# Kernel optimization log

Hardware: AMD Instinct MI355X
Metric: run time of the kernel (lower is better)

The kernel has to match this reference:

```python
import jax, jax.numpy as jnp
import numpy as np

EPS = 1e-8  # torch cosine_similarity default eps


def setup_inputs() -> dict:
    key = jax.random.key(0)
    x = jax.random.normal(key, (256, 200, 1024), dtype=jnp.float32)
    return {"x": x}


def reference(x):
    # x: [B, c, l]
    # Cosine-similarity Gram matrix, fused: dot(i,j) / max(||x_i||*||x_j||, eps)
    norms = jnp.linalg.norm(x, axis=-1)                      # [B, c]
    dots = jnp.einsum('bil,bjl->bij', x, x)                  # [B, c, c]
    sim = dots / jnp.maximum(norms[:, :, None] * norms[:, None, :], EPS)
    atten = jax.nn.softmax(sim, axis=-1)                     # [B, c, c]
    out = jnp.einsum('bij,bjl->bil', atten, x) + x           # bmm + residual
    return out
```

## Files before the change

kernel.cpp:

```cpp
#include <hip/hip_runtime.h>
#include <math.h>


typedef unsigned int uint32;
typedef __attribute__((ext_vector_type(8))) short bf16x8;
typedef __attribute__((ext_vector_type(4))) float f32x4;
typedef __attribute__((ext_vector_type(4))) uint32 u32x4;

#define CC 200
#define LL 1024
#define EPSV 1e-8f

__device__ __forceinline__ uint32 bfb(float f) {
  uint32 u = __float_as_uint(f);
  u += 0x7fffu + ((u >> 16) & 1u);
  return u >> 16;
}

__global__ __launch_bounds__(512, 2)
void spe_attn_kernel(const float* __restrict__ x, float* __restrict__ out) {
  const int tid  = threadIdx.x;
  const int lane = tid & 63;
  const int w    = tid >> 6;
  const int lm   = lane & 15;
  const int lg   = lane >> 4;
  const int bidx = blockIdx.x;
  const float* xb = x + (size_t)bidx * (CC * LL);
  float* ob       = out + (size_t)bidx * (CC * LL);

  __shared__ uint32 LDS[39120];
  uint32* pl    = LDS;
  uint32* xa0   = LDS + 24128;
  uint32* xa1   = LDS + 31616;
  uint32* xbuf  = LDS + 24128;
  float*  norms = (float*)(LDS + 38912);

  const bool two = (w < 5);
  const int rb0 = w;
  const int rb1 = two ? (w + 8) : w;

  const f32x4 fz = {0.f, 0.f, 0.f, 0.f};
  f32x4 acc[2][13];
  #pragma unroll
  for (int i = 0; i < 2; ++i)
    #pragma unroll
    for (int j = 0; j < 13; ++j) acc[i][j] = fz;

  if (tid < 288) { xa0[7200 + tid] = 0u; xa1[7200 + tid] = 0u; }

  float4 vst[7];
  #pragma unroll
  for (int i = 0; i < 7; ++i) {
    int idx = tid + i * 512;
    if (idx < 3200) {
      int row = idx >> 4, c4 = idx & 15;
      vst[i] = *(const float4*)(xb + row * LL + c4 * 4);
    }
  }
  #pragma unroll
  for (int i = 0; i < 7; ++i) {
    int idx = tid + i * 512;
    if (idx < 3200) {
      int row = idx >> 4, c4 = idx & 15;
      uint2 wv;
      wv.x = bfb(vst[i].x) | (bfb(vst[i].y) << 16);
      wv.y = bfb(vst[i].z) | (bfb(vst[i].w) << 16);
      *(uint2*)&xa0[row * 36 + c4 * 2] = wv;
    }
  }

  for (int s = 0; s < 16; ++s) {
    __syncthreads();
    if (s + 1 < 16) {
      #pragma unroll
      for (int i = 0; i < 7; ++i) {
        int idx = tid + i * 512;
        if (idx < 3200) {
          int row = idx >> 4, c4 = idx & 15;
          vst[i] = *(const float4*)(xb + row * LL + (s + 1) * 64 + c4 * 4);
        }
      }
    }
    const uint32* cur = (s & 1) ? xa1 : xa0;
    #pragma unroll
    for (int ks = 0; ks < 2; ++ks) {
      bf16x8 a0 = *(const bf16x8*)&cur[(rb0 * 16 + lm) * 36 + ks * 16 + lg * 4];
      bf16x8 a1 = a0;
      if (two) a1 = *(const bf16x8*)&cur[(rb1 * 16 + lm) * 36 + ks * 16 + lg * 4];
      #pragma unroll
      for (int ct = 0; ct < 13; ++ct) {
        bf16x8 bf = *(const bf16x8*)&cur[(ct * 16 + lm) * 36 + ks * 16 + lg * 4];
        acc[0][ct] = __builtin_amdgcn_mfma_f32_16x16x32_bf16(a0, bf, acc[0][ct], 0, 0, 0);
        if (two)
          acc[1][ct] = __builtin_amdgcn_mfma_f32_16x16x32_bf16(a1, bf, acc[1][ct], 0, 0, 0);
      }
    }
    if (s + 1 < 16) {
      uint32* nxt = (s & 1) ? xa0 : xa1;
      #pragma unroll
      for (int i = 0; i < 7; ++i) {
        int idx = tid + i * 512;
        if (idx < 3200) {
          int row = idx >> 4, c4 = idx & 15;
          uint2 wv;
          wv.x = bfb(vst[i].x) | (bfb(vst[i].y) << 16);
          wv.y = bfb(vst[i].z) | (bfb(vst[i].w) << 16);
          *(uint2*)&nxt[row * 36 + c4 * 2] = wv;
        }
      }
    }
  }

  #pragma unroll
  for (int rbi = 0; rbi < 2; ++rbi) {
    if (rbi == 0 || two) {
      int rb = rbi ? rb1 : rb0;
      #pragma unroll
      for (int ct = 0; ct < 13; ++ct) {
        if (ct == rb) {
          #pragma unroll
          for (int r = 0; r < 4; ++r) {
            int ri = lg * 4 + r;
            if (lm == ri) norms[rb * 16 + ri] = sqrtf(acc[rbi][ct][r]);
          }
        }
      }
    }
  }
  __syncthreads();

  float cn[13];
  #pragma unroll
  for (int ct = 0; ct < 13; ++ct) cn[ct] = norms[ct * 16 + lm];

  #pragma unroll
  for (int rbi = 0; rbi < 2; ++rbi) {
    if (rbi == 0 || two) {
      int rb = rbi ? rb1 : rb0;
      #pragma unroll
      for (int r = 0; r < 4; ++r) {
        int grow = rb * 16 + lg * 4 + r;
        float rn = norms[grow];
        float sv[13];
        float m = -INFINITY;
        #pragma unroll
        for (int ct = 0; ct < 13; ++ct) {
          int gc = ct * 16 + lm;
          float sval = acc[rbi][ct][r] / fmaxf(rn * cn[ct], EPSV);
          sval = (gc < CC) ? sval : -INFINITY;
          sv[ct] = sval;
          m = fmaxf(m, sval);
        }
        #pragma unroll
        for (int off = 1; off < 16; off <<= 1) m = fmaxf(m, __shfl_xor(m, off));
        float sum = 0.f;
        #pragma unroll
        for (int ct = 0; ct < 13; ++ct) {
          float e = __expf(sv[ct] - m);
          sv[ct] = e;
          sum += e;
        }
        #pragma unroll
        for (int off = 1; off < 16; off <<= 1) sum += __shfl_xor(sum, off);
        float inv = 1.0f / sum;
        #pragma unroll
        for (int ct = 0; ct < 13; ++ct) {
          int gc = ct * 16 + lm;
          float p = sv[ct] * inv + ((gc == grow) ? 1.0f : 0.0f);
          uint32 pb = bfb(p);
          uint32 qb = (uint32)__shfl_xor((int)pb, 1);
          if (!(lane & 1)) pl[grow * 116 + ct * 8 + (lm >> 1)] = pb | (qb << 16);
        }
      }
      for (int i = lane; i < 256; i += 64)
        pl[(rb * 16 + (i >> 4)) * 116 + 100 + (i & 15)] = 0u;
    }
  }

  for (int nc = 0; nc < 8; ++nc) {
    const int n0 = nc * 128;
    __syncthreads();
    #pragma unroll
    for (int pass = 0; pass < 14; ++pass) {
      int kp = pass * 8 + w;
      int r0 = kp * 2, r1 = r0 + 1;
      int n = n0 + (lane << 1);
      float2 va = (r0 < CC) ? *(const float2*)(xb + r0 * LL + n) : make_float2(0.f, 0.f);
      float2 vb = (r1 < CC) ? *(const float2*)(xb + r1 * LL + n) : make_float2(0.f, 0.f);
      uint2 wv;
      wv.x = bfb(va.x) | (bfb(vb.x) << 16);
      wv.y = bfb(va.y) | (bfb(vb.y) << 16);
      *(uint2*)&xbuf[kp * 132 + (lane << 1)] = wv;
    }
    __syncthreads();

    f32x4 acc2[2][8];
    #pragma unroll
    for (int i = 0; i < 2; ++i)
      #pragma unroll
      for (int j = 0; j < 8; ++j) acc2[i][j] = fz;

    #pragma unroll
    for (int ks = 0; ks < 7; ++ks) {
      bf16x8 a0 = *(const bf16x8*)&pl[(rb0 * 16 + lm) * 116 + ks * 16 + lg * 4];
      bf16x8 a1 = a0;
      if (two) a1 = *(const bf16x8*)&pl[(rb1 * 16 + lm) * 116 + ks * 16 + lg * 4];
      #pragma unroll
      for (int ct = 0; ct < 8; ++ct) {
        int kpb = ks * 16 + lg * 4;
        int col = ct * 16 + lm;
        u32x4 bv;
        bv[0] = xbuf[(kpb + 0) * 132 + col];
        bv[1] = xbuf[(kpb + 1) * 132 + col];
        bv[2] = xbuf[(kpb + 2) * 132 + col];
        bv[3] = xbuf[(kpb + 3) * 132 + col];
        bf16x8 bf = __builtin_bit_cast(bf16x8, bv);
        acc2[0][ct] = __builtin_amdgcn_mfma_f32_16x16x32_bf16(a0, bf, acc2[0][ct], 0, 0, 0);
        if (two)
          acc2[1][ct] = __builtin_amdgcn_mfma_f32_16x16x32_bf16(a1, bf, acc2[1][ct], 0, 0, 0);
      }
    }

    #pragma unroll
    for (int rbi = 0; rbi < 2; ++rbi) {
      if (rbi == 0 || two) {
        int rb = rbi ? rb1 : rb0;
        #pragma unroll
        for (int ct = 0; ct < 8; ++ct) {
          #pragma unroll
          for (int r = 0; r < 4; ++r) {
            int grow = rb * 16 + lg * 4 + r;
            if (grow < CC) ob[grow * LL + n0 + ct * 16 + lm] = acc2[rbi][ct][r];
          }
        }
      }
    }
  }
}

extern "C" void kernel_launch(void* const* d_in, const int* in_sizes, int n_in,
                              void* d_out, int out_size, void* d_ws, size_t ws_size,
                              hipStream_t stream) {
  const float* x = (const float*)d_in[0];
  float* out = (float*)d_out;
  const int B = in_sizes[0] / (CC * LL);
  spe_attn_kernel<<<dim3(B), dim3(512), 0, stream>>>(x, out);
}
```

Baseline: 164.0 us.

## Split each batch across two blocks by row tiles to raise occupancy

Each batch is now handled by two blocks, each owning about half of the 13 row tiles of the Gram matrix. One spare wave computes the diagonal tiles the other half needs for the norms. Shared memory shrinks (single-buffered x tile, norms packed into padding of the probability buffer), which allows launch bounds of 4 blocks per CU and keeps A fragments of P in registers. The second GEMM uses a transposed, XOR-swizzled bf16 buffer with 128-bit LDS reads over 64-column chunks. In exchange, the Gram pass redundantly loads and converts the full x in both blocks and adds an extra barrier per k-step, and the column chunk loop now does 16 narrower scalar global loads.

```diff
diff --git a/kernel.cpp b/kernel.cpp
--- a/kernel.cpp
+++ b/kernel.cpp
@@ -5,11 +5,13 @@
 typedef unsigned int uint32;
 typedef __attribute__((ext_vector_type(8))) short bf16x8;
 typedef __attribute__((ext_vector_type(4))) float f32x4;
-typedef __attribute__((ext_vector_type(4))) uint32 u32x4;
 
 #define CC 200
 #define LL 1024
 #define EPSV 1e-8f
+#define PLSTR 116
+#define XASTR 36
+#define XBSTR 116
 
 __device__ __forceinline__ uint32 bfb(float f) {
   uint32 u = __float_as_uint(f);
@@ -17,7 +19,7 @@
   return u >> 16;
 }
 
-__global__ __launch_bounds__(512, 2)
+__global__ __launch_bounds__(512, 4)
 void spe_attn_kernel(const float* __restrict__ x, float* __restrict__ out) {
   const int tid  = threadIdx.x;
   const int lane = tid & 63;
@@ -25,28 +27,28 @@
   const int lm   = lane & 15;
   const int lg   = lane >> 4;
   const int bidx = blockIdx.x;
-  const float* xb = x + (size_t)bidx * (CC * LL);
-  float* ob       = out + (size_t)bidx * (CC * LL);
-
-  __shared__ uint32 LDS[39120];
-  uint32* pl    = LDS;
-  uint32* xa0   = LDS + 24128;
-  uint32* xa1   = LDS + 31616;
-  uint32* xbuf  = LDS + 24128;
-  float*  norms = (float*)(LDS + 38912);
-
-  const bool two = (w < 5);
-  const int rb0 = w;
-  const int rb1 = two ? (w + 8) : w;
+  const int batch = bidx >> 1;
+  const int half  = bidx & 1;
+  const float* xb = x + (size_t)batch * (CC * LL);
+  float* ob       = out + (size_t)batch * (CC * LL);
+
+  const int hb     = half ? 7 : 0;
+  const int ntiles = half ? 6 : 7;
+  const int dbase  = half ? 0 : 7;
+  const int ndiag  = 13 - ntiles;
+
+  __shared__ uint32 LDS[20480];
+  uint32* pl   = LDS;
+  uint32* xa   = LDS + 12992;
+  uint32* xbuf = LDS + 12992;
+  #define NRM(g) (*(float*)&pl[((g) >> 1) * PLSTR + 112 + ((g) & 1)])
 
   const f32x4 fz = {0.f, 0.f, 0.f, 0.f};
-  f32x4 acc[2][13];
+  f32x4 acc[13];
   #pragma unroll
-  for (int i = 0; i < 2; ++i)
-    #pragma unroll
-    for (int j = 0; j < 13; ++j) acc[i][j] = fz;
-
-  if (tid < 288) { xa0[7200 + tid] = 0u; xa1[7200 + tid] = 0u; }
+  for (int j = 0; j < 13; ++j) acc[j] = fz;
+
+  if (tid < 288) xa[7200 + tid] = 0u;
 
   float4 vst[7];
   #pragma unroll
@@ -65,7 +67,7 @@
       uint2 wv;
       wv.x = bfb(vst[i].x) | (bfb(vst[i].y) << 16);
       wv.y = bfb(vst[i].z) | (bfb(vst[i].w) << 16);
-      *(uint2*)&xa0[row * 36 + c4 * 2] = wv;
+      *(uint2*)&xa[row * XASTR + c4 * 2] = wv;
     }
   }
 
@@ -81,22 +83,27 @@
         }
       }
     }
-    const uint32* cur = (s & 1) ? xa1 : xa0;
     #pragma unroll
     for (int ks = 0; ks < 2; ++ks) {
-      bf16x8 a0 = *(const bf16x8*)&cur[(rb0 * 16 + lm) * 36 + ks * 16 + lg * 4];
-      bf16x8 a1 = a0;
-      if (two) a1 = *(const bf16x8*)&cur[(rb1 * 16 + lm) * 36 + ks * 16 + lg * 4];
-      #pragma unroll
-      for (int ct = 0; ct < 13; ++ct) {
-        bf16x8 bf = *(const bf16x8*)&cur[(ct * 16 + lm) * 36 + ks * 16 + lg * 4];
-        acc[0][ct] = __builtin_amdgcn_mfma_f32_16x16x32_bf16(a0, bf, acc[0][ct], 0, 0, 0);
-        if (two)
-          acc[1][ct] = __builtin_amdgcn_mfma_f32_16x16x32_bf16(a1, bf, acc[1][ct], 0, 0, 0);
-      }
-    }
+      if (w < ntiles) {
+        bf16x8 a = *(const bf16x8*)&xa[((hb + w) * 16 + lm) * XASTR + ks * 16 + lg * 4];
+        #pragma unroll
+        for (int ct = 0; ct < 13; ++ct) {
+          bf16x8 b = *(const bf16x8*)&xa[(ct * 16 + lm) * XASTR + ks * 16 + lg * 4];
+          acc[ct] = __builtin_amdgcn_mfma_f32_16x16x32_bf16(a, b, acc[ct], 0, 0, 0);
+        }
+      } else if (w == ntiles) {
+        #pragma unroll
+        for (int d = 0; d < 7; ++d) {
+          if (d < ndiag) {
+            bf16x8 f = *(const bf16x8*)&xa[((dbase + d) * 16 + lm) * XASTR + ks * 16 + lg * 4];
+            acc[d] = __builtin_amdgcn_mfma_f32_16x16x32_bf16(f, f, acc[d], 0, 0, 0);
+          }
+        }
+      }
+    }
+    __syncthreads();
     if (s + 1 < 16) {
-      uint32* nxt = (s & 1) ? xa0 : xa1;
       #pragma unroll
       for (int i = 0; i < 7; ++i) {
         int idx = tid + i * 512;
@@ -105,137 +112,130 @@
           uint2 wv;
           wv.x = bfb(vst[i].x) | (bfb(vst[i].y) << 16);
           wv.y = bfb(vst[i].z) | (bfb(vst[i].w) << 16);
-          *(uint2*)&nxt[row * 36 + c4 * 2] = wv;
-        }
-      }
-    }
-  }
-
-  #pragma unroll
-  for (int rbi = 0; rbi < 2; ++rbi) {
-    if (rbi == 0 || two) {
-      int rb = rbi ? rb1 : rb0;
+          *(uint2*)&xa[row * XASTR + c4 * 2] = wv;
+        }
+      }
+    }
+  }
+
+  if (w < ntiles) {
+    const int t = hb + w;
+    #pragma unroll
+    for (int ct = 0; ct < 13; ++ct) {
+      if (ct == t) {
+        #pragma unroll
+        for (int r = 0; r < 4; ++r) {
+          int ri = lg * 4 + r;
+          if (lm == ri) NRM(t * 16 + ri) = sqrtf(acc[ct][r]);
+        }
+      }
+    }
+  } else if (w == ntiles) {
+    #pragma unroll
+    for (int d = 0; d < 7; ++d) {
+      if (d < ndiag) {
+        int t = dbase + d;
+        #pragma unroll
+        for (int r = 0; r < 4; ++r) {
+          int ri = lg * 4 + r;
+          if (lm == ri) NRM(t * 16 + ri) = sqrtf(acc[d][r]);
+        }
+      }
+    }
+  }
+  __syncthreads();
+
+  bf16x8 pa[7];
+  if (w < ntiles) {
+    float cn[13];
+    #pragma unroll
+    for (int ct = 0; ct < 13; ++ct) cn[ct] = NRM(ct * 16 + lm);
+
+    #pragma unroll
+    for (int r = 0; r < 4; ++r) {
+      int grow = (hb + w) * 16 + lg * 4 + r;
+      int lrow = w * 16 + lg * 4 + r;
+      float rn = NRM(grow);
+      float sv[13];
+      float m = -INFINITY;
       #pragma unroll
       for (int ct = 0; ct < 13; ++ct) {
-        if (ct == rb) {
-          #pragma unroll
-          for (int r = 0; r < 4; ++r) {
-            int ri = lg * 4 + r;
-            if (lm == ri) norms[rb * 16 + ri] = sqrtf(acc[rbi][ct][r]);
-          }
-        }
-      }
-    }
-  }
-  __syncthreads();
-
-  float cn[13];
-  #pragma unroll
-  for (int ct = 0; ct < 13; ++ct) cn[ct] = norms[ct * 16 + lm];
-
-  #pragma unroll
-  for (int rbi = 0; rbi < 2; ++rbi) {
-    if (rbi == 0 || two) {
-      int rb = rbi ? rb1 : rb0;
-      #pragma unroll
-      for (int r = 0; r < 4; ++r) {
-        int grow = rb * 16 + lg * 4 + r;
-        float rn = norms[grow];
-        float sv[13];
-        float m = -INFINITY;
-        #pragma unroll
-        for (int ct = 0; ct < 13; ++ct) {
-          int gc = ct * 16 + lm;
-          float sval = acc[rbi][ct][r] / fmaxf(rn * cn[ct], EPSV);
-          sval = (gc < CC) ? sval : -INFINITY;
-          sv[ct] = sval;
-          m = fmaxf(m, sval);
-        }
-        #pragma unroll
-        for (int off = 1; off < 16; off <<= 1) m = fmaxf(m, __shfl_xor(m, off));
-        float sum = 0.f;
-        #pragma unroll
-        for (int ct = 0; ct < 13; ++ct) {
-          float e = __expf(sv[ct] - m);
-          sv[ct] = e;
-          sum += e;
-        }
-        #pragma unroll
-        for (int off = 1; off < 16; off <<= 1) sum += __shfl_xor(sum, off);
-        float inv = 1.0f / sum;
-        #pragma unroll
-        for (int ct = 0; ct < 13; ++ct) {
-          int gc = ct * 16 + lm;
-          float p = sv[ct] * inv + ((gc == grow) ? 1.0f : 0.0f);
-          uint32 pb = bfb(p);
-          uint32 qb = (uint32)__shfl_xor((int)pb, 1);
-          if (!(lane & 1)) pl[grow * 116 + ct * 8 + (lm >> 1)] = pb | (qb << 16);
-        }
-      }
-      for (int i = lane; i < 256; i += 64)
-        pl[(rb * 16 + (i >> 4)) * 116 + 100 + (i & 15)] = 0u;
-    }
-  }
-
-  for (int nc = 0; nc < 8; ++nc) {
-    const int n0 = nc * 128;
+        int gc = ct * 16 + lm;
+        float sval = acc[ct][r] / fmaxf(rn * cn[ct], EPSV);
+        sval = (gc < CC) ? sval : -INFINITY;
+        sv[ct] = sval;
+        m = fmaxf(m, sval);
+      }
+      #pragma unroll
+      for (int off = 1; off < 16; off <<= 1) m = fmaxf(m, __shfl_xor(m, off));
+      float sum = 0.f;
+      #pragma unroll
+      for (int ct = 0; ct < 13; ++ct) {
+        float e = __expf(sv[ct] - m);
+        sv[ct] = e;
+        sum += e;
+      }
+      #pragma unroll
+      for (int off = 1; off < 16; off <<= 1) sum += __shfl_xor(sum, off);
+      float inv = 1.0f / sum;
+      #pragma unroll
+      for (int ct = 0; ct < 13; ++ct) {
+        int gc = ct * 16 + lm;
+        float p = sv[ct] * inv + ((gc == grow) ? 1.0f : 0.0f);
+        uint32 pb = bfb(p);
+        uint32 qb = (uint32)__shfl_xor((int)pb, 1);
+        if (!(lane & 1)) pl[lrow * PLSTR + ct * 8 + (lm >> 1)] = pb | (qb << 16);
+      }
+    }
+    #pragma unroll
+    for (int i = 0; i < 4; ++i) {
+      int idx = lane + i * 64;
+      int rr = idx >> 4, c = idx & 15;
+      if (c < 12) pl[(w * 16 + rr) * PLSTR + 100 + c] = 0u;
+    }
+    #pragma unroll
+    for (int ks = 0; ks < 7; ++ks)
+      pa[ks] = *(const bf16x8*)&pl[(w * 16 + lm) * PLSTR + ks * 16 + lg * 4];
+  }
+
+  for (int nc = 0; nc < 16; ++nc) {
+    const int n0 = nc * 64;
     __syncthreads();
     #pragma unroll
     for (int pass = 0; pass < 14; ++pass) {
       int kp = pass * 8 + w;
       int r0 = kp * 2, r1 = r0 + 1;
-      int n = n0 + (lane << 1);
-      float2 va = (r0 < CC) ? *(const float2*)(xb + r0 * LL + n) : make_float2(0.f, 0.f);
-      float2 vb = (r1 < CC) ? *(const float2*)(xb + r1 * LL + n) : make_float2(0.f, 0.f);
-      uint2 wv;
-      wv.x = bfb(va.x) | (bfb(vb.x) << 16);
-      wv.y = bfb(va.y) | (bfb(vb.y) << 16);
-      *(uint2*)&xbuf[kp * 132 + (lane << 1)] = wv;
-    }
-    __syncthreads();
-
-    f32x4 acc2[2][8];
-    #pragma unroll
-    for (int i = 0; i < 2; ++i)
-      #pragma unroll
-      for (int j = 0; j < 8; ++j) acc2[i][j] = fz;
-
-    #pragma unroll
-    for (int ks = 0; ks < 7; ++ks) {
-      bf16x8 a0 = *(const bf16x8*)&pl[(rb0 * 16 + lm) * 116 + ks * 16 + lg * 4];
-      bf16x8 a1 = a0;
-      if (two) a1 = *(const bf16x8*)&pl[(rb1 * 16 + lm) * 116 + ks * 16 + lg * 4];
-      #pragma unroll
-      for (int ct = 0; ct < 8; ++ct) {
-        int kpb = ks * 16 + lg * 4;
-        int col = ct * 16 + lm;
-        u32x4 bv;
-        bv[0] = xbuf[(kpb + 0) * 132 + col];
-        bv[1] = xbuf[(kpb + 1) * 132 + col];
-        bv[2] = xbuf[(kpb + 2) * 132 + col];
-        bv[3] = xbuf[(kpb + 3) * 132 + col];
-        bf16x8 bf = __builtin_bit_cast(bf16x8, bv);
-        acc2[0][ct] = __builtin_amdgcn_mfma_f32_16x16x32_bf16(a0, bf, acc2[0][ct], 0, 0, 0);
-        if (two)
-          acc2[1][ct] = __builtin_amdgcn_mfma_f32_16x16x32_bf16(a1, bf, acc2[1][ct], 0, 0, 0);
-      }
-    }
-
-    #pragma unroll
-    for (int rbi = 0; rbi < 2; ++rbi) {
-      if (rbi == 0 || two) {
-        int rb = rbi ? rb1 : rb0;
-        #pragma unroll
-        for (int ct = 0; ct < 8; ++ct) {
-          #pragma unroll
-          for (int r = 0; r < 4; ++r) {
-            int grow = rb * 16 + lg * 4 + r;
-            if (grow < CC) ob[grow * LL + n0 + ct * 16 + lm] = acc2[rbi][ct][r];
-          }
-        }
-      }
-    }
-  }
+      float va = (r0 < CC) ? xb[r0 * LL + n0 + lane] : 0.f;
+      float vb = (r1 < CC) ? xb[r1 * LL + n0 + lane] : 0.f;
+      int sw = ((lane >> 3) & 3) << 2;
+      xbuf[lane * XBSTR + (kp ^ sw)] = bfb(va) | (bfb(vb) << 16);
+    }
+    __syncthreads();
+
+    if (w < ntiles) {
+      f32x4 acc2[4] = {fz, fz, fz, fz};
+      #pragma unroll
+      for (int ks = 0; ks < 7; ++ks) {
+        #pragma unroll
+        for (int ct = 0; ct < 4; ++ct) {
+          int col = ct * 16 + lm;
+          int kpb = ks * 16 + lg * 4;
+          int sw = ((col >> 3) & 3) << 2;
+          bf16x8 b = *(const bf16x8*)&xbuf[col * XBSTR + (kpb ^ sw)];
+          acc2[ct] = __builtin_amdgcn_mfma_f32_16x16x32_bf16(pa[ks], b, acc2[ct], 0, 0, 0);
+        }
+      }
+      #pragma unroll
+      for (int ct = 0; ct < 4; ++ct) {
+        #pragma unroll
+        for (int r = 0; r < 4; ++r) {
+          int grow = (hb + w) * 16 + lg * 4 + r;
+          if (grow < CC) ob[grow * LL + n0 + ct * 16 + lm] = acc2[ct][r];
+        }
+      }
+    }
+  }
+  #undef NRM
 }
 
 extern "C" void kernel_launch(void* const* d_in, const int* in_sizes, int n_in,
@@ -244,5 +244,5 @@
   const float* x = (const float*)d_in[0];
   float* out = (float*)d_out;
   const int B = in_sizes[0] / (CC * LL);
-  spe_attn_kernel<<<dim3(B), dim3(512), 0, stream>>>(x, out);
+  spe_attn_kernel<<<dim3(2 * B), dim3(512), 0, stream>>>(x, out);
 }
```

Result: slower. 258.1 us (+57.3%).

## Prefetch x chunks into registers, transpose xbuf, and hoist P fragments

Applied to the files above, without the earlier changes.

The second GEMM (attention times x) now loads each next 64-column chunk of x into registers while the current chunk is being computed. The chunk is stored into LDS transposed (column-major with stride 132), so each B fragment becomes one 128-bit LDS read instead of four scalar reads. The attention A-fragments are loaded into registers once instead of every iteration. This adds register pressure, so launch bounds drop to one block per CU and the chunk width is halved, which doubles the number of chunk iterations and barriers.

```diff
diff --git a/kernel.cpp b/kernel.cpp
--- a/kernel.cpp
+++ b/kernel.cpp
@@ -5,11 +5,13 @@
 typedef unsigned int uint32;
 typedef __attribute__((ext_vector_type(8))) short bf16x8;
 typedef __attribute__((ext_vector_type(4))) float f32x4;
-typedef __attribute__((ext_vector_type(4))) uint32 u32x4;
 
 #define CC 200
 #define LL 1024
 #define EPSV 1e-8f
+#define PLSTR 116
+#define XASTR 36
+#define XBSTR 132
 
 __device__ __forceinline__ uint32 bfb(float f) {
   uint32 u = __float_as_uint(f);
@@ -17,7 +19,7 @@
   return u >> 16;
 }
 
-__global__ __launch_bounds__(512, 2)
+__global__ __launch_bounds__(512, 1)
 void spe_attn_kernel(const float* __restrict__ x, float* __restrict__ out) {
   const int tid  = threadIdx.x;
   const int lane = tid & 63;
@@ -28,12 +30,12 @@
   const float* xb = x + (size_t)bidx * (CC * LL);
   float* ob       = out + (size_t)bidx * (CC * LL);
 
-  __shared__ uint32 LDS[39120];
+  __shared__ uint32 LDS[39312];
   uint32* pl    = LDS;
   uint32* xa0   = LDS + 24128;
   uint32* xa1   = LDS + 31616;
   uint32* xbuf  = LDS + 24128;
-  float*  norms = (float*)(LDS + 38912);
+  float*  norms = (float*)(LDS + 39104);
 
   const bool two = (w < 5);
   const int rb0 = w;
@@ -65,7 +67,7 @@
       uint2 wv;
       wv.x = bfb(vst[i].x) | (bfb(vst[i].y) << 16);
       wv.y = bfb(vst[i].z) | (bfb(vst[i].w) << 16);
-      *(uint2*)&xa0[row * 36 + c4 * 2] = wv;
+      *(uint2*)&xa0[row * XASTR + c4 * 2] = wv;
     }
   }
 
@@ -84,12 +86,12 @@
     const uint32* cur = (s & 1) ? xa1 : xa0;
     #pragma unroll
     for (int ks = 0; ks < 2; ++ks) {
-      bf16x8 a0 = *(const bf16x8*)&cur[(rb0 * 16 + lm) * 36 + ks * 16 + lg * 4];
+      bf16x8 a0 = *(const bf16x8*)&cur[(rb0 * 16 + lm) * XASTR + ks * 16 + lg * 4];
       bf16x8 a1 = a0;
-      if (two) a1 = *(const bf16x8*)&cur[(rb1 * 16 + lm) * 36 + ks * 16 + lg * 4];
+      if (two) a1 = *(const bf16x8*)&cur[(rb1 * 16 + lm) * XASTR + ks * 16 + lg * 4];
       #pragma unroll
       for (int ct = 0; ct < 13; ++ct) {
-        bf16x8 bf = *(const bf16x8*)&cur[(ct * 16 + lm) * 36 + ks * 16 + lg * 4];
+        bf16x8 bf = *(const bf16x8*)&cur[(ct * 16 + lm) * XASTR + ks * 16 + lg * 4];
         acc[0][ct] = __builtin_amdgcn_mfma_f32_16x16x32_bf16(a0, bf, acc[0][ct], 0, 0, 0);
         if (two)
           acc[1][ct] = __builtin_amdgcn_mfma_f32_16x16x32_bf16(a1, bf, acc[1][ct], 0, 0, 0);
@@ -105,7 +107,7 @@
           uint2 wv;
           wv.x = bfb(vst[i].x) | (bfb(vst[i].y) << 16);
           wv.y = bfb(vst[i].z) | (bfb(vst[i].w) << 16);
-          *(uint2*)&nxt[row * 36 + c4 * 2] = wv;
+          *(uint2*)&nxt[row * XASTR + c4 * 2] = wv;
         }
       }
     }
@@ -169,55 +171,67 @@
           float p = sv[ct] * inv + ((gc == grow) ? 1.0f : 0.0f);
           uint32 pb = bfb(p);
           uint32 qb = (uint32)__shfl_xor((int)pb, 1);
-          if (!(lane & 1)) pl[grow * 116 + ct * 8 + (lm >> 1)] = pb | (qb << 16);
-        }
-      }
-      for (int i = lane; i < 256; i += 64)
-        pl[(rb * 16 + (i >> 4)) * 116 + 100 + (i & 15)] = 0u;
-    }
-  }
-
-  for (int nc = 0; nc < 8; ++nc) {
-    const int n0 = nc * 128;
+          if (!(lane & 1)) pl[grow * PLSTR + ct * 8 + (lm >> 1)] = pb | (qb << 16);
+        }
+      }
+      for (int i = lane; i < 256; i += 64) {
+        int rr = i >> 4, c = i & 15;
+        if (c < 12) pl[(rb * 16 + rr) * PLSTR + 100 + c] = 0u;
+      }
+    }
+  }
+
+  bf16x8 pa[2][7];
+  #pragma unroll
+  for (int ks = 0; ks < 7; ++ks) {
+    pa[0][ks] = *(const bf16x8*)&pl[(rb0 * 16 + lm) * PLSTR + ks * 16 + lg * 4];
+    if (two)
+      pa[1][ks] = *(const bf16x8*)&pl[(rb1 * 16 + lm) * PLSTR + ks * 16 + lg * 4];
+  }
+
+  float pva[14], pvb[14];
+  #pragma unroll
+  for (int p = 0; p < 14; ++p) {
+    int kp = p * 8 + w;
+    int r0 = kp * 2, r1 = r0 + 1;
+    pva[p] = (r0 < CC) ? xb[r0 * LL + lane] : 0.f;
+    pvb[p] = (r1 < CC) ? xb[r1 * LL + lane] : 0.f;
+  }
+
+  for (int nc = 0; nc < 16; ++nc) {
+    const int n0 = nc * 64;
     __syncthreads();
     #pragma unroll
-    for (int pass = 0; pass < 14; ++pass) {
-      int kp = pass * 8 + w;
-      int r0 = kp * 2, r1 = r0 + 1;
-      int n = n0 + (lane << 1);
-      float2 va = (r0 < CC) ? *(const float2*)(xb + r0 * LL + n) : make_float2(0.f, 0.f);
-      float2 vb = (r1 < CC) ? *(const float2*)(xb + r1 * LL + n) : make_float2(0.f, 0.f);
-      uint2 wv;
-      wv.x = bfb(va.x) | (bfb(vb.x) << 16);
-      wv.y = bfb(va.y) | (bfb(vb.y) << 16);
-      *(uint2*)&xbuf[kp * 132 + (lane << 1)] = wv;
+    for (int p = 0; p < 14; ++p) {
+      int kp = p * 8 + w;
+      xbuf[lane * XBSTR + kp] = bfb(pva[p]) | (bfb(pvb[p]) << 16);
     }
     __syncthreads();
-
-    f32x4 acc2[2][8];
+    if (nc + 1 < 16) {
+      const int n1 = (nc + 1) * 64;
+      #pragma unroll
+      for (int p = 0; p < 14; ++p) {
+        int kp = p * 8 + w;
+        int r0 = kp * 2, r1 = r0 + 1;
+        pva[p] = (r0 < CC) ? xb[r0 * LL + n1 + lane] : 0.f;
+        pvb[p] = (r1 < CC) ? xb[r1 * LL + n1 + lane] : 0.f;
+      }
+    }
+
+    f32x4 acc2[2][4];
     #pragma unroll
     for (int i = 0; i < 2; ++i)
       #pragma unroll
-      for (int j = 0; j < 8; ++j) acc2[i][j] = fz;
+      for (int j = 0; j < 4; ++j) acc2[i][j] = fz;
 
     #pragma unroll
     for (int ks = 0; ks < 7; ++ks) {
-      bf16x8 a0 = *(const bf16x8*)&pl[(rb0 * 16 + lm) * 116 + ks * 16 + lg * 4];
-      bf16x8 a1 = a0;
-      if (two) a1 = *(const bf16x8*)&pl[(rb1 * 16 + lm) * 116 + ks * 16 + lg * 4];
-      #pragma unroll
-      for (int ct = 0; ct < 8; ++ct) {
-        int kpb = ks * 16 + lg * 4;
-        int col = ct * 16 + lm;
-        u32x4 bv;
-        bv[0] = xbuf[(kpb + 0) * 132 + col];
-        bv[1] = xbuf[(kpb + 1) * 132 + col];
-        bv[2] = xbuf[(kpb + 2) * 132 + col];
-        bv[3] = xbuf[(kpb + 3) * 132 + col];
-        bf16x8 bf = __builtin_bit_cast(bf16x8, bv);
-        acc2[0][ct] = __builtin_amdgcn_mfma_f32_16x16x32_bf16(a0, bf, acc2[0][ct], 0, 0, 0);
+      #pragma unroll
+      for (int ct = 0; ct < 4; ++ct) {
+        bf16x8 b = *(const bf16x8*)&xbuf[(ct * 16 + lm) * XBSTR + ks * 16 + lg * 4];
+        acc2[0][ct] = __builtin_amdgcn_mfma_f32_16x16x32_bf16(pa[0][ks], b, acc2[0][ct], 0, 0, 0);
         if (two)
-          acc2[1][ct] = __builtin_amdgcn_mfma_f32_16x16x32_bf16(a1, bf, acc2[1][ct], 0, 0, 0);
+          acc2[1][ct] = __builtin_amdgcn_mfma_f32_16x16x32_bf16(pa[1][ks], b, acc2[1][ct], 0, 0, 0);
       }
     }
 
@@ -226,7 +240,7 @@
       if (rbi == 0 || two) {
         int rb = rbi ? rb1 : rb0;
         #pragma unroll
-        for (int ct = 0; ct < 8; ++ct) {
+        for (int ct = 0; ct < 4; ++ct) {
           #pragma unroll
           for (int r = 0; r < 4; ++r) {
             int grow = rb * 16 + lg * 4 + r;
```

Result: faster. 157.5 us (-4.0%).
